# Performance work log

Measured on AMD Instinct MI355X. Metric: run time of the kernel, lower is better.

## Reference

```python
import jax, jax.numpy as jnp
import numpy as np

NEG_SLOPE = 0.2  # PyG GATConv default leaky_relu slope


def _gat_conv(x, src, dst, W, a_src, a_dst, b, num_nodes):
    # Linear transform: [N, F_out]
    h = x @ W
    # Per-node attention halves (heads=1): [N]
    alpha_s = h @ a_src
    alpha_d = h @ a_dst
    # Per-edge raw score for edge j->i: a_src.h_j + a_dst.h_i
    e = jax.nn.leaky_relu(alpha_s[src] + alpha_d[dst], NEG_SLOPE)
    # Softmax over edges grouped by destination node (numerically stable)
    m = jax.ops.segment_max(e, dst, num_segments=num_nodes)
    ex = jnp.exp(e - m[dst])
    denom = jax.ops.segment_sum(ex, dst, num_segments=num_nodes)
    coef = ex / denom[dst]
    # Attention-weighted aggregation of source features into destinations
    out = jax.ops.segment_sum(h[src] * coef[:, None], dst, num_segments=num_nodes)
    return out + b


def setup_inputs() -> dict:
    key = jax.random.key(0)
    ks = jax.random.split(key, 12)
    N, F_in, F_hid, F_out, E = 100000, 128, 64, 40, 1600000
    x = jax.random.normal(ks[0], (N, F_in), dtype=jnp.float32)
    edge_index = jax.random.randint(ks[1], (2, E), 0, N, dtype=jnp.int64)
    g = lambda k, shape, fan: jax.random.normal(k, shape, dtype=jnp.float32) * (1.0 / np.sqrt(fan))
    return {
        "x": x,
        "edge_index": edge_index,
        "W1": g(ks[2], (F_in, F_hid), F_in),
        "a_src1": g(ks[3], (F_hid,), F_hid),
        "a_dst1": g(ks[4], (F_hid,), F_hid),
        "b1": jnp.zeros((F_hid,), dtype=jnp.float32),
        "W2": g(ks[5], (F_hid, F_out), F_hid),
        "a_src2": g(ks[6], (F_out,), F_out),
        "a_dst2": g(ks[7], (F_out,), F_out),
        "b2": jnp.zeros((F_out,), dtype=jnp.float32),
    }


def reference(x, edge_index, W1, a_src1, a_dst1, b1, W2, a_src2, a_dst2, b2):
    N = x.shape[0]
    # PyG GATConv adds self loops by default
    loops = jnp.arange(N, dtype=edge_index.dtype)
    src = jnp.concatenate([edge_index[0], loops])
    dst = jnp.concatenate([edge_index[1], loops])
    h = _gat_conv(x, src, dst, W1, a_src1, a_dst1, b1, N)
    h = jax.nn.relu(h)
    # dropout p=0.5 is inactive in eval mode
    h = _gat_conv(h, src, dst, W2, a_src2, a_dst2, b2, N)
    return jax.nn.log_softmax(h, axis=-1)
```

## Files before the change

### kernel.cpp

```cpp
#include <hip/hip_runtime.h>
#include <math.h>


constexpr int F_IN = 128;
constexpr int F_H  = 64;
constexpr int F_O  = 40;
constexpr int NBMAX = 512;
constexpr int CHUNK = 8192;

using h2 = decltype(__builtin_amdgcn_cvt_pkrtz(0.f, 0.f));

__device__ __forceinline__ h2 u2h(unsigned u) { return __builtin_bit_cast(h2, u); }
__device__ __forceinline__ unsigned h2u(h2 h) { return __builtin_bit_cast(unsigned, h); }

__device__ __forceinline__ float fdot2f(h2 a, h2 b, float c) {
#if __has_builtin(__builtin_amdgcn_fdot2)
    return __builtin_amdgcn_fdot2(a, b, c, false);
#else
    return c + (float)a.x * (float)b.x + (float)a.y * (float)b.y;
#endif
}
__device__ __forceinline__ h2 pklo(unsigned a, unsigned b) {
    return u2h(__builtin_amdgcn_perm(a, b, 0x05040100u));
}
__device__ __forceinline__ h2 pkhi(unsigned a, unsigned b) {
    return u2h(__builtin_amdgcn_perm(a, b, 0x07060302u));
}
__device__ __forceinline__ unsigned short f2h(float f) {
    _Float16 x = (_Float16)f;
    return __builtin_bit_cast(unsigned short, x);
}


__global__ __launch_bounds__(256) void k_binA(const int* __restrict__ dsts,
                                              int* __restrict__ bcnt,
                                              int E, int Et, int NB) {
    __shared__ int hist[NBMAX];
    for (int i = threadIdx.x; i < NB; i += 256) hist[i] = 0;
    __syncthreads();
    int e0 = blockIdx.x * 2048;
#pragma unroll
    for (int it = 0; it < 8; ++it) {
        int e = e0 + it * 256 + threadIdx.x;
        if (e < Et) {
            int d = (e < E) ? dsts[e] : (e - E);
            atomicAdd(&hist[d >> 8], 1);
        }
    }
    __syncthreads();
    for (int i = threadIdx.x; i < NB; i += 256) {
        int c = hist[i];
        if (c) atomicAdd(&bcnt[i], c);
    }
}

__global__ __launch_bounds__(NBMAX) void k_binB(const int* __restrict__ bcnt,
                                                int* __restrict__ bbase,
                                                int* __restrict__ bcur,
                                                int* __restrict__ rp,
                                                int NB, int N, int Et) {
    __shared__ int sc[NBMAX];
    int t = threadIdx.x;
    int v = (t < NB) ? bcnt[t] : 0;
    sc[t] = v; __syncthreads();
    int x = v;
    for (int o = 1; o < NBMAX; o <<= 1) {
        int y = (t >= o) ? sc[t - o] : 0;
        __syncthreads();
        x += y;
        sc[t] = x;
        __syncthreads();
    }
    if (t < NB) { int b = x - v; bbase[t] = b; bcur[t] = b; }
    if (t == 0) rp[N] = Et;
}

__global__ __launch_bounds__(256) void k_binC(const int* __restrict__ srcs,
                                              const int* __restrict__ dsts,
                                              int* __restrict__ bcur,
                                              unsigned* __restrict__ binned,
                                              int E, int Et, int NB) {
    __shared__ int hist[NBMAX];
    __shared__ int gbase[NBMAX];
    __shared__ int lcnt[NBMAX];
    int t = threadIdx.x;
    for (int i = t; i < NB; i += 256) hist[i] = 0;
    __syncthreads();
    int e0 = blockIdx.x * CHUNK;
#pragma unroll 4
    for (int it = 0; it < CHUNK / 256; ++it) {
        int e = e0 + it * 256 + t;
        if (e < Et) {
            int d = (e < E) ? dsts[e] : (e - E);
            atomicAdd(&hist[d >> 8], 1);
        }
    }
    __syncthreads();
    for (int i = t; i < NB; i += 256) {
        int c = hist[i];
        gbase[i] = c ? atomicAdd(&bcur[i], c) : 0;
        lcnt[i] = 0;
    }
    __syncthreads();
#pragma unroll 4
    for (int it = 0; it < CHUNK / 256; ++it) {
        int e = e0 + it * 256 + t;
        if (e < Et) {
            int s, d;
            if (e < E) { s = srcs[e]; d = dsts[e]; } else { s = e - E; d = s; }
            int b = d >> 8;
            int p = atomicAdd(&lcnt[b], 1);
            binned[gbase[b] + p] = (unsigned)s | ((unsigned)(d & 255) << 24);
        }
    }
}

__global__ __launch_bounds__(256) void k_binD(const unsigned* __restrict__ binned,
                                              const int* __restrict__ bbase,
                                              const int* __restrict__ bcur,
                                              int* __restrict__ rp,
                                              int* __restrict__ csr, int N) {
    __shared__ int hist[256];
    __shared__ int sc[256];
    __shared__ int lcnt[256];
    int b = blockIdx.x, t = threadIdx.x;
    int base = bbase[b], end = bcur[b];
    hist[t] = 0; __syncthreads();
    for (int j = base + t; j < end; j += 256)
        atomicAdd(&hist[binned[j] >> 24], 1);
    __syncthreads();
    int v = hist[t];
    sc[t] = v; __syncthreads();
    int x = v;
    for (int o = 1; o < 256; o <<= 1) {
        int y = (t >= o) ? sc[t - o] : 0;
        __syncthreads();
        x += y;
        sc[t] = x;
        __syncthreads();
    }
    int pref = x - v;
    int g = (b << 8) + t;
    if (g < N) rp[g] = base + pref;
    sc[t] = pref;
    lcnt[t] = 0;
    __syncthreads();
    for (int j = base + t; j < end; j += 256) {
        unsigned w = binned[j];
        int v2 = (int)(w >> 24);
        int s = (int)(w & 0xFFFFFFu);
        int p = atomicAdd(&lcnt[v2], 1);
        csr[base + sc[v2] + p] = s;
    }
}


__global__ __launch_bounds__(256) void k_gemm1(const float* __restrict__ x,
                                               const float* __restrict__ W,
                                               const float* __restrict__ avs,
                                               const float* __restrict__ avd,
                                               unsigned short* __restrict__ h,
                                               float* __restrict__ as,
                                               float* __restrict__ ad, int N) {
    __shared__ __align__(16) float Ws[F_IN * F_H];
    for (int i = threadIdx.x; i < F_IN * F_H; i += 256) Ws[i] = W[i];
    __syncthreads();
    int t = threadIdx.x;
    int r0 = blockIdx.x * 64 + (t >> 4) * 4;
    int c0 = (t & 15) * 4;
    if (r0 >= N) return;
    const float* xp = x + (size_t)r0 * F_IN;
    float acc[4][4] = {};
    for (int k4 = 0; k4 < F_IN / 4; ++k4) {
        int kb = k4 * 4;
        float4 w0 = *(const float4*)&Ws[(kb + 0) * F_H + c0];
        float4 w1 = *(const float4*)&Ws[(kb + 1) * F_H + c0];
        float4 w2 = *(const float4*)&Ws[(kb + 2) * F_H + c0];
        float4 w3 = *(const float4*)&Ws[(kb + 3) * F_H + c0];
#pragma unroll
        for (int r = 0; r < 4; ++r) {
            float4 xv = *(const float4*)&xp[(size_t)r * F_IN + kb];
            acc[r][0] += xv.x * w0.x + xv.y * w1.x + xv.z * w2.x + xv.w * w3.x;
            acc[r][1] += xv.x * w0.y + xv.y * w1.y + xv.z * w2.y + xv.w * w3.y;
            acc[r][2] += xv.x * w0.z + xv.y * w1.z + xv.z * w2.z + xv.w * w3.z;
            acc[r][3] += xv.x * w0.w + xv.y * w1.w + xv.z * w2.w + xv.w * w3.w;
        }
    }
    float4 avs4 = *(const float4*)&avs[c0];
    float4 avd4 = *(const float4*)&avd[c0];
#pragma unroll
    for (int r = 0; r < 4; ++r) {
        unsigned lo = h2u(__builtin_amdgcn_cvt_pkrtz(acc[r][0], acc[r][1]));
        unsigned hi = h2u(__builtin_amdgcn_cvt_pkrtz(acc[r][2], acc[r][3]));
        ((uint2*)h)[((size_t)(r0 + r) * F_H + c0) >> 2] = make_uint2(lo, hi);
        float ps = acc[r][0] * avs4.x + acc[r][1] * avs4.y + acc[r][2] * avs4.z + acc[r][3] * avs4.w;
        float pd = acc[r][0] * avd4.x + acc[r][1] * avd4.y + acc[r][2] * avd4.z + acc[r][3] * avd4.w;
#pragma unroll
        for (int o = 8; o; o >>= 1) {
            ps += __shfl_xor(ps, o, 16);
            pd += __shfl_xor(pd, o, 16);
        }
        if ((t & 15) == 0) { as[r0 + r] = ps; ad[r0 + r] = pd; }
    }
}


__global__ __launch_bounds__(256) void k_gemm2(const float* __restrict__ xin,
                                               const float* __restrict__ W,
                                               const float* __restrict__ avs,
                                               const float* __restrict__ avd,
                                               unsigned short* __restrict__ h,
                                               float* __restrict__ as,
                                               float* __restrict__ ad, int N) {
    __shared__ __align__(16) float Ws[F_H * F_O];
    for (int i = threadIdx.x; i < F_H * F_O; i += 256) Ws[i] = W[i];
    __syncthreads();
    int t = threadIdx.x;
    int r0 = blockIdx.x * 64 + (t >> 3) * 2;
    int l = t & 7;
    if (r0 >= N) return;
    const float4* xa = (const float4*)(xin + (size_t)r0 * F_H);
    const float4* xb = (const float4*)(xin + (size_t)(r0 + 1) * F_H);
    float acca[5] = {}, accb[5] = {};
#pragma unroll
    for (int k4 = 0; k4 < F_H / 4; ++k4) {
        float4 xva = xa[k4];
        float4 xvb = xb[k4];
        int kb = k4 * 4;
#pragma unroll
        for (int kk = 0; kk < 4; ++kk) {
            const float* wr = &Ws[(kb + kk) * F_O + l];
            float w0 = wr[0], w1 = wr[8], w2 = wr[16], w3 = wr[24], w4 = wr[32];
            float xs = (&xva.x)[kk];
            acca[0] += xs * w0; acca[1] += xs * w1; acca[2] += xs * w2;
            acca[3] += xs * w3; acca[4] += xs * w4;
            float ys = (&xvb.x)[kk];
            accb[0] += ys * w0; accb[1] += ys * w1; accb[2] += ys * w2;
            accb[3] += ys * w3; accb[4] += ys * w4;
        }
    }
    float psa = 0.f, pda = 0.f, psb = 0.f, pdb = 0.f;
    unsigned short* ra = h + (size_t)r0 * F_H;
    unsigned short* rb = h + (size_t)(r0 + 1) * F_H;
#pragma unroll
    for (int cc = 0; cc < 5; ++cc) {
        int c = l + 8 * cc;
        ra[c] = f2h(acca[cc]);
        rb[c] = f2h(accb[cc]);
        float vs = avs[c], vd = avd[c];
        psa += acca[cc] * vs; pda += acca[cc] * vd;
        psb += accb[cc] * vs; pdb += accb[cc] * vd;
    }
#pragma unroll
    for (int pp = 0; pp < 3; ++pp) {
        int c = 40 + l * 3 + pp;
        ra[c] = 0; rb[c] = 0;
    }
#pragma unroll
    for (int o = 4; o; o >>= 1) {
        psa += __shfl_xor(psa, o, 8);
        pda += __shfl_xor(pda, o, 8);
        psb += __shfl_xor(psb, o, 8);
        pdb += __shfl_xor(pdb, o, 8);
    }
    if (l == 0) { as[r0] = psa; ad[r0] = pda; as[r0 + 1] = psb; ad[r0 + 1] = pdb; }
}


template <int FOUT, bool RELU, bool LOGSM>
__global__ __launch_bounds__(256) void k_agg(const int* __restrict__ rp,
                                             const int* __restrict__ csr,
                                             const float* __restrict__ as,
                                             const float* __restrict__ ad,
                                             const uint4* __restrict__ h4,
                                             const float* __restrict__ bias,
                                             float* __restrict__ out, int N) {
    constexpr int CAP = 64;
    __shared__ __align__(16) uint2 wsb[4][8][CAP + 2];
    const int w = threadIdx.x >> 6;
    const int g = (threadIdx.x >> 3) & 7;
    const int c = threadIdx.x & 7;
    const int i = blockIdx.x * 32 + (threadIdx.x >> 3);
    if (i >= N) return;
    const int start = rp[i], end = rp[i + 1];
    const int deg = end - start;
    const int dm = min(deg, CAP);
    const float adi = ad[i];

    for (int idx = c; idx < dm; idx += 8) {
        int srcn = csr[start + idx];
        float e = as[srcn] + adi;
        e = fmaxf(e, 0.2f * e);
        wsb[w][g][idx] = make_uint2(__float_as_uint(__expf(e)), (unsigned)srcn);
    }
    if (c == 0 && (dm & 1))
        wsb[w][g][dm] = make_uint2(0u, (unsigned)i);

    const uint4* pw = (const uint4*)wsb[w][g];
    float acc[8] = {};
    float sacc = 0.f;
    const int npair = (dm + 1) >> 1;
    for (int p = 0; p < npair; ++p) {
        uint4 t = pw[p];
        float w0 = __uint_as_float(t.x), w1 = __uint_as_float(t.z);
        sacc += w0 + w1;
        uint4 hv0 = h4[((unsigned)t.y << 3) + c];
        uint4 hv1 = h4[((unsigned)t.w << 3) + c];
        h2 wp = __builtin_amdgcn_cvt_pkrtz(w0, w1);
        acc[0] = fdot2f(wp, pklo(hv1.x, hv0.x), acc[0]);
        acc[1] = fdot2f(wp, pkhi(hv1.x, hv0.x), acc[1]);
        acc[2] = fdot2f(wp, pklo(hv1.y, hv0.y), acc[2]);
        acc[3] = fdot2f(wp, pkhi(hv1.y, hv0.y), acc[3]);
        acc[4] = fdot2f(wp, pklo(hv1.z, hv0.z), acc[4]);
        acc[5] = fdot2f(wp, pkhi(hv1.z, hv0.z), acc[5]);
        acc[6] = fdot2f(wp, pklo(hv1.w, hv0.w), acc[6]);
        acc[7] = fdot2f(wp, pkhi(hv1.w, hv0.w), acc[7]);
    }

    for (int j = start + dm; j < end; ++j) {
        int srcn = csr[j];
        float e = as[srcn] + adi;
        e = fmaxf(e, 0.2f * e);
        float wv = __expf(e);
        sacc += wv;
        uint4 hv = h4[((unsigned)srcn << 3) + c];
        h2 wp = __builtin_amdgcn_cvt_pkrtz(wv, 0.f);
        acc[0] = fdot2f(wp, pklo(hv.x, hv.x), acc[0]);
        acc[1] = fdot2f(wp, pkhi(hv.x, hv.x), acc[1]);
        acc[2] = fdot2f(wp, pklo(hv.y, hv.y), acc[2]);
        acc[3] = fdot2f(wp, pkhi(hv.y, hv.y), acc[3]);
        acc[4] = fdot2f(wp, pklo(hv.z, hv.z), acc[4]);
        acc[5] = fdot2f(wp, pkhi(hv.z, hv.z), acc[5]);
        acc[6] = fdot2f(wp, pklo(hv.w, hv.w), acc[6]);
        acc[7] = fdot2f(wp, pkhi(hv.w, hv.w), acc[7]);
    }

    float inv = 1.f / sacc;

    if (!LOGSM) {
        float r[8];
#pragma unroll
        for (int k = 0; k < 8; ++k) {
            r[k] = fmaf(acc[k], inv, bias[8 * c + k]);
            if (RELU) r[k] = fmaxf(r[k], 0.f);
        }
        float4* op = (float4*)(out + (size_t)i * FOUT + 8 * c);
        op[0] = make_float4(r[0], r[1], r[2], r[3]);
        op[1] = make_float4(r[4], r[5], r[6], r[7]);
    } else {
        constexpr int VC = FOUT / 8;
        bool act = (c < VC);
        float v[8];
#pragma unroll
        for (int k = 0; k < 8; ++k) {
            float bv = bias[act ? 8 * c + k : 0];
            v[k] = act ? fmaf(acc[k], inv, bv) : -INFINITY;
        }
        float mx = v[0];
#pragma unroll
        for (int k = 1; k < 8; ++k) mx = fmaxf(mx, v[k]);
#pragma unroll
        for (int o = 1; o <= 4; o <<= 1) mx = fmaxf(mx, __shfl_xor(mx, o));
        float es = 0.f;
        if (act) {
#pragma unroll
            for (int k = 0; k < 8; ++k) es += __expf(v[k] - mx);
        }
#pragma unroll
        for (int o = 1; o <= 4; o <<= 1) es += __shfl_xor(es, o);
        if (act) {
            float lse = mx + __logf(es);
            float4* op = (float4*)(out + (size_t)i * FOUT + 8 * c);
            op[0] = make_float4(v[0] - lse, v[1] - lse, v[2] - lse, v[3] - lse);
            op[1] = make_float4(v[4] - lse, v[5] - lse, v[6] - lse, v[7] - lse);
        }
    }
}


extern "C" void kernel_launch(void* const* d_in, const int* in_sizes, int n_in,
                              void* d_out, int out_size, void* d_ws, size_t ws_size,
                              hipStream_t stream) {
    const float* x   = (const float*)d_in[0];
    const int* edges = (const int*)d_in[1];
    const float* W1  = (const float*)d_in[2];
    const float* av_s1 = (const float*)d_in[3];
    const float* av_d1 = (const float*)d_in[4];
    const float* b1  = (const float*)d_in[5];
    const float* W2  = (const float*)d_in[6];
    const float* av_s2 = (const float*)d_in[7];
    const float* av_d2 = (const float*)d_in[8];
    const float* b2  = (const float*)d_in[9];
    float* out = (float*)d_out;

    const int N  = in_sizes[0] / F_IN;
    const int E  = in_sizes[1] / 2;
    const int Et = E + N;
    const int NB = (N + 255) >> 8;

    char* p = (char*)d_ws;
    auto alloc = [&](size_t bytes) {
        char* q = p;
        p += (bytes + 255) & ~(size_t)255;
        return (void*)q;
    };
    unsigned short* h1 = (unsigned short*)alloc((size_t)N * F_H * 2);
    float* out1   = (float*)alloc((size_t)N * F_H * 4);
    float* as1    = (float*)alloc((size_t)N * 4);
    float* ad1    = (float*)alloc((size_t)N * 4);
    float* as2    = (float*)alloc((size_t)N * 4);
    float* ad2    = (float*)alloc((size_t)N * 4);
    int* rp       = (int*)alloc((size_t)(N + 1) * 4);
    int* bcnt     = (int*)alloc(NBMAX * 4);
    int* bbase    = (int*)alloc(NBMAX * 4);
    int* bcur     = (int*)alloc(NBMAX * 4);
    unsigned* binned = (unsigned*)alloc((size_t)Et * 4);
    int* csr      = (int*)alloc((size_t)Et * 4);
    (void)n_in; (void)out_size; (void)ws_size;

    const int* srcs = edges;
    const int* dsts = edges + E;

    hipMemsetAsync(bcnt, 0, NBMAX * 4, stream);

    k_binA<<<(Et + 2047) / 2048, 256, 0, stream>>>(dsts, bcnt, E, Et, NB);
    k_binB<<<1, NBMAX, 0, stream>>>(bcnt, bbase, bcur, rp, NB, N, Et);
    k_binC<<<(Et + CHUNK - 1) / CHUNK, 256, 0, stream>>>(srcs, dsts, bcur, binned, E, Et, NB);
    k_binD<<<NB, 256, 0, stream>>>(binned, bbase, bcur, rp, csr, N);

    k_gemm1<<<(N + 63) / 64, 256, 0, stream>>>(x, W1, av_s1, av_d1, h1, as1, ad1, N);
    int gAgg = (N + 31) / 32;
    k_agg<F_H, true, false><<<gAgg, 256, 0, stream>>>(rp, csr, as1, ad1,
                                                      (const uint4*)h1, b1, out1, N);
    k_gemm2<<<(N + 63) / 64, 256, 0, stream>>>(out1, W2, av_s2, av_d2, h1, as2, ad2, N);
    k_agg<F_O, false, true><<<gAgg, 256, 0, stream>>>(rp, csr, as2, ad2,
                                                      (const uint4*)h1, b2, out, N);
}
```

Baseline: 307.9 us.

## Use split-bf16 MFMA for first-layer GEMM with transposed weight prep kernel

```diff
diff --git a/kernel.cpp b/kernel.cpp
--- a/kernel.cpp
+++ b/kernel.cpp
@@ -9,9 +9,10 @@
 constexpr int CHUNK = 8192;
 
 using h2 = decltype(__builtin_amdgcn_cvt_pkrtz(0.f, 0.f));
+typedef __attribute__((ext_vector_type(4))) float f32x4;
+typedef __attribute__((ext_vector_type(8))) short s16x8;
 
 __device__ __forceinline__ h2 u2h(unsigned u) { return __builtin_bit_cast(h2, u); }
-__device__ __forceinline__ unsigned h2u(h2 h) { return __builtin_bit_cast(unsigned, h); }
 
 __device__ __forceinline__ float fdot2f(h2 a, h2 b, float c) {
 #if __has_builtin(__builtin_amdgcn_fdot2)
@@ -155,52 +156,112 @@
 }
 
 
-__global__ __launch_bounds__(256) void k_gemm1(const float* __restrict__ x,
-                                               const float* __restrict__ W,
-                                               const float* __restrict__ avs,
-                                               const float* __restrict__ avd,
-                                               unsigned short* __restrict__ h,
-                                               float* __restrict__ as,
-                                               float* __restrict__ ad, int N) {
-    __shared__ __align__(16) float Ws[F_IN * F_H];
-    for (int i = threadIdx.x; i < F_IN * F_H; i += 256) Ws[i] = W[i];
-    __syncthreads();
-    int t = threadIdx.x;
-    int r0 = blockIdx.x * 64 + (t >> 4) * 4;
-    int c0 = (t & 15) * 4;
-    if (r0 >= N) return;
-    const float* xp = x + (size_t)r0 * F_IN;
-    float acc[4][4] = {};
-    for (int k4 = 0; k4 < F_IN / 4; ++k4) {
-        int kb = k4 * 4;
-        float4 w0 = *(const float4*)&Ws[(kb + 0) * F_H + c0];
-        float4 w1 = *(const float4*)&Ws[(kb + 1) * F_H + c0];
-        float4 w2 = *(const float4*)&Ws[(kb + 2) * F_H + c0];
-        float4 w3 = *(const float4*)&Ws[(kb + 3) * F_H + c0];
-#pragma unroll
-        for (int r = 0; r < 4; ++r) {
-            float4 xv = *(const float4*)&xp[(size_t)r * F_IN + kb];
-            acc[r][0] += xv.x * w0.x + xv.y * w1.x + xv.z * w2.x + xv.w * w3.x;
-            acc[r][1] += xv.x * w0.y + xv.y * w1.y + xv.z * w2.y + xv.w * w3.y;
-            acc[r][2] += xv.x * w0.z + xv.y * w1.z + xv.z * w2.z + xv.w * w3.z;
-            acc[r][3] += xv.x * w0.w + xv.y * w1.w + xv.z * w2.w + xv.w * w3.w;
-        }
-    }
-    float4 avs4 = *(const float4*)&avs[c0];
-    float4 avd4 = *(const float4*)&avd[c0];
+__global__ __launch_bounds__(256) void k_wsplit(const float* __restrict__ W,
+                                                unsigned short* __restrict__ WhiT,
+                                                unsigned short* __restrict__ WloT) {
+    int i = blockIdx.x * 256 + threadIdx.x;
+    if (i >= F_IN * F_H) return;
+    int k = i >> 6, c = i & 63;
+    float w = W[i];
+    unsigned u = __float_as_uint(w);
+    unsigned hi = u & 0xFFFF0000u;
+    float d = w - __uint_as_float(hi);
+    WhiT[c * F_IN + k] = (unsigned short)(hi >> 16);
+    WloT[c * F_IN + k] = (unsigned short)(__float_as_uint(d) >> 16);
+}
+
+
+__global__ __launch_bounds__(256) void k_gemm1m(const float* __restrict__ x,
+                                                const unsigned short* __restrict__ WhiT,
+                                                const unsigned short* __restrict__ WloT,
+                                                const float* __restrict__ avs,
+                                                const float* __restrict__ avd,
+                                                unsigned short* __restrict__ h,
+                                                float* __restrict__ as,
+                                                float* __restrict__ ad, int N) {
+    __shared__ unsigned short hs[64][72];
+    const int t = threadIdx.x;
+    const int wv = t >> 6;
+    const int lane = t & 63;
+    const int lrow = lane & 15;
+    const int lk8 = lane >> 4;
+    const int r0 = blockIdx.x * 64;
+    const int arow = r0 + wv * 16 + lrow;
+    const float* xp = x + (size_t)min(arow, N - 1) * F_IN;
+
+    float4 xv0[4], xv1[4];
+#pragma unroll
+    for (int kt = 0; kt < 4; ++kt) {
+        xv0[kt] = *(const float4*)&xp[kt * 32 + lk8 * 8];
+        xv1[kt] = *(const float4*)&xp[kt * 32 + lk8 * 8 + 4];
+    }
+    s16x8 ah[4], al[4];
+#pragma unroll
+    for (int kt = 0; kt < 4; ++kt) {
+        float e0[8] = {xv0[kt].x, xv0[kt].y, xv0[kt].z, xv0[kt].w,
+                       xv1[kt].x, xv1[kt].y, xv1[kt].z, xv1[kt].w};
+        unsigned uh[4], ul[4];
+#pragma unroll
+        for (int p = 0; p < 4; ++p) {
+            float a0 = e0[2 * p], a1 = e0[2 * p + 1];
+            unsigned u0 = __float_as_uint(a0), u1 = __float_as_uint(a1);
+            float d0 = a0 - __uint_as_float(u0 & 0xFFFF0000u);
+            float d1 = a1 - __uint_as_float(u1 & 0xFFFF0000u);
+            uh[p] = __builtin_amdgcn_perm(u1, u0, 0x07060302u);
+            ul[p] = __builtin_amdgcn_perm(__float_as_uint(d1), __float_as_uint(d0), 0x07060302u);
+        }
+        ah[kt] = __builtin_bit_cast(s16x8, make_uint4(uh[0], uh[1], uh[2], uh[3]));
+        al[kt] = __builtin_bit_cast(s16x8, make_uint4(ul[0], ul[1], ul[2], ul[3]));
+    }
+
+    f32x4 acc[4] = {};
+#pragma unroll
+    for (int kt = 0; kt < 4; ++kt) {
+#pragma unroll
+        for (int ct = 0; ct < 4; ++ct) {
+            const int boff = (ct * 16 + lrow) * F_IN + kt * 32 + lk8 * 8;
+            s16x8 bh = *(const s16x8*)&WhiT[boff];
+            s16x8 bl = *(const s16x8*)&WloT[boff];
+            acc[ct] = __builtin_amdgcn_mfma_f32_16x16x32_bf16(ah[kt], bh, acc[ct], 0, 0, 0);
+            acc[ct] = __builtin_amdgcn_mfma_f32_16x16x32_bf16(al[kt], bh, acc[ct], 0, 0, 0);
+            acc[ct] = __builtin_amdgcn_mfma_f32_16x16x32_bf16(ah[kt], bl, acc[ct], 0, 0, 0);
+        }
+    }
+
+    float avs_c[4], avd_c[4];
+#pragma unroll
+    for (int ct = 0; ct < 4; ++ct) {
+        avs_c[ct] = avs[ct * 16 + lrow];
+        avd_c[ct] = avd[ct * 16 + lrow];
+    }
 #pragma unroll
     for (int r = 0; r < 4; ++r) {
-        unsigned lo = h2u(__builtin_amdgcn_cvt_pkrtz(acc[r][0], acc[r][1]));
-        unsigned hi = h2u(__builtin_amdgcn_cvt_pkrtz(acc[r][2], acc[r][3]));
-        ((uint2*)h)[((size_t)(r0 + r) * F_H + c0) >> 2] = make_uint2(lo, hi);
-        float ps = acc[r][0] * avs4.x + acc[r][1] * avs4.y + acc[r][2] * avs4.z + acc[r][3] * avs4.w;
-        float pd = acc[r][0] * avd4.x + acc[r][1] * avd4.y + acc[r][2] * avd4.z + acc[r][3] * avd4.w;
+        float ps = acc[0][r] * avs_c[0] + acc[1][r] * avs_c[1]
+                 + acc[2][r] * avs_c[2] + acc[3][r] * avs_c[3];
+        float pd = acc[0][r] * avd_c[0] + acc[1][r] * avd_c[1]
+                 + acc[2][r] * avd_c[2] + acc[3][r] * avd_c[3];
 #pragma unroll
         for (int o = 8; o; o >>= 1) {
             ps += __shfl_xor(ps, o, 16);
             pd += __shfl_xor(pd, o, 16);
         }
-        if ((t & 15) == 0) { as[r0 + r] = ps; ad[r0 + r] = pd; }
+        int orow = r0 + wv * 16 + lk8 * 4 + r;
+        if (lrow == 0 && orow < N) { as[orow] = ps; ad[orow] = pd; }
+    }
+
+#pragma unroll
+    for (int ct = 0; ct < 4; ++ct)
+#pragma unroll
+        for (int r = 0; r < 4; ++r)
+            hs[wv * 16 + lk8 * 4 + r][ct * 16 + lrow] = f2h(acc[ct][r]);
+    __syncthreads();
+    const int row = t >> 2, ch = t & 3;
+    const int grow = r0 + row;
+    if (grow < N) {
+        uint4 v0 = *(const uint4*)&hs[row][ch * 16];
+        uint4 v1 = *(const uint4*)&hs[row][ch * 16 + 8];
+        uint4* gp = (uint4*)(h + (size_t)grow * F_H + ch * 16);
+        gp[0] = v0; gp[1] = v1;
     }
 }
 
@@ -416,6 +477,8 @@
     int* bcur     = (int*)alloc(NBMAX * 4);
     unsigned* binned = (unsigned*)alloc((size_t)Et * 4);
     int* csr      = (int*)alloc((size_t)Et * 4);
+    unsigned short* WhiT = (unsigned short*)alloc((size_t)F_H * F_IN * 2);
+    unsigned short* WloT = (unsigned short*)alloc((size_t)F_H * F_IN * 2);
     (void)n_in; (void)out_size; (void)ws_size;
 
     const int* srcs = edges;
@@ -423,12 +486,13 @@
 
     hipMemsetAsync(bcnt, 0, NBMAX * 4, stream);
 
+    k_wsplit<<<(F_IN * F_H + 255) / 256, 256, 0, stream>>>(W1, WhiT, WloT);
     k_binA<<<(Et + 2047) / 2048, 256, 0, stream>>>(dsts, bcnt, E, Et, NB);
     k_binB<<<1, NBMAX, 0, stream>>>(bcnt, bbase, bcur, rp, NB, N, Et);
     k_binC<<<(Et + CHUNK - 1) / CHUNK, 256, 0, stream>>>(srcs, dsts, bcur, binned, E, Et, NB);
     k_binD<<<NB, 256, 0, stream>>>(binned, bbase, bcur, rp, csr, N);
 
-    k_gemm1<<<(N + 63) / 64, 256, 0, stream>>>(x, W1, av_s1, av_d1, h1, as1, ad1, N);
+    k_gemm1m<<<(N + 63) / 64, 256, 0, stream>>>(x, WhiT, WloT, av_s1, av_d1, h1, as1, ad1, N);
     int gAgg = (N + 31) / 32;
     k_agg<F_H, true, false><<<gAgg, 256, 0, stream>>>(rp, csr, as1, ad1,
                                                       (const uint4*)h1, b1, out1, N);
```

Result: faster. 296.0 us (-3.9%).
